# Kernel optimization log

Measured on AMD Instinct MI355X. Metric: run time of the kernel, lower is better.

## Reference

```python
import jax, jax.numpy as jnp
import numpy as np

N_NODES = 50000
N_EDGES = 800000
IN, HID, OUT = 256, 128, 64


def setup_inputs() -> dict:
    key = jax.random.key(0)
    ks = jax.random.split(key, 5)
    return {
        "x": jax.random.normal(ks[0], (N_NODES, IN), dtype=jnp.float32),
        "W1": jax.random.normal(ks[1], (IN, HID), dtype=jnp.float32) / np.sqrt(IN),
        "b1": jnp.zeros((HID,), dtype=jnp.float32),
        "W2": jax.random.normal(ks[2], (HID, OUT), dtype=jnp.float32) / np.sqrt(HID),
        "b2": jnp.zeros((OUT,), dtype=jnp.float32),
        "src": jax.random.randint(ks[3], (N_EDGES,), 0, N_NODES, dtype=jnp.int32),
        "dst": jax.random.randint(ks[4], (N_EDGES,), 0, N_NODES, dtype=jnp.int32),
    }


def _graph_conv(h, W, b, src, dst, norm_src, norm_dst, n_nodes):
    # DGL GraphConv, norm='both': y = D_dst^{-1/2} A D_src^{-1/2} h W + b
    # Project first (smaller feature dim for the SpMM), linearity makes it exact.
    h = h @ W                                     # [N, d_out]
    msg = (h * norm_src[:, None])[src]            # gather per-edge   [E, d_out]
    agg = jax.ops.segment_sum(msg, dst, num_segments=n_nodes)  # [N, d_out]
    return agg * norm_dst[:, None] + b


def reference(x, W1, b1, W2, b2, src, dst):
    n = x.shape[0]
    ones = jnp.ones(src.shape[0], dtype=jnp.float32)
    out_deg = jnp.zeros(n, jnp.float32).at[src].add(ones)
    in_deg = jnp.zeros(n, jnp.float32).at[dst].add(ones)
    norm_src = jax.lax.rsqrt(jnp.maximum(out_deg, 1.0))
    norm_dst = jax.lax.rsqrt(jnp.maximum(in_deg, 1.0))

    h = _graph_conv(x, W1, b1, src, dst, norm_src, norm_dst, n)
    h = jax.nn.relu(h)
    return _graph_conv(h, W2, b2, src, dst, norm_src, norm_dst, n)
```

## Files before the change

### kernel.cpp

```cpp
#include <hip/hip_runtime.h>

#define NN 50000
#define NE 800000
#define NPAD 50176
#define NSLICE 32
#define ESL 25000
#define HPN 25088
#define HPW 12544
#define FPN 12544
#define GB 782

typedef __attribute__((ext_vector_type(8))) short bf16x8;
typedef __attribute__((ext_vector_type(4))) float f32x4;

__device__ __forceinline__ float u2f(unsigned u) { return __uint_as_float(u); }
__device__ __forceinline__ unsigned f2u(float f) { return __float_as_uint(f); }
__device__ __forceinline__ unsigned short f2bf(float f) {
    unsigned u = f2u(f);
    return (unsigned short)((u + (((u >> 16) & 1u) + 0x7fffu)) >> 16);
}

__global__ __launch_bounds__(256) void wtrans_kernel(
    const float* __restrict__ W1, const float* __restrict__ W2,
    unsigned short* __restrict__ Wh1, unsigned short* __restrict__ Wl1,
    unsigned short* __restrict__ Wh2, unsigned short* __restrict__ Wl2) {
    int b = blockIdx.x;
    float w;
    unsigned short *ph, *pl;
    int f;
    if (b < 128) {
        int i = b * 256 + threadIdx.x;
        int k = i >> 7, n = i & 127;
        f = (((n >> 4) * 32 + (k >> 3)) * 16 + (n & 15)) * 8 + (k & 7);
        w = W1[i]; ph = Wh1; pl = Wl1;
    } else {
        int i = (b - 128) * 256 + threadIdx.x;
        int k = i >> 6, n = i & 63;
        f = (((n >> 4) * 16 + (k >> 3)) * 16 + (n & 15)) * 8 + (k & 7);
        w = W2[i]; ph = Wh2; pl = Wl2;
    }
    unsigned u = f2u(w);
    float lo = w - u2f(u & 0xffff0000u);
    ph[f] = (unsigned short)(u >> 16);
    pl[f] = (unsigned short)(f2u(lo) >> 16);
}

__global__ __launch_bounds__(1024) void hist_kernel(
    const int* __restrict__ src, const int* __restrict__ dst,
    unsigned* __restrict__ cnt_sl) {
    __shared__ unsigned lcnt[HPW];
    const int b = blockIdx.x;
    const int side = b & 1;
    const int slice = (b >> 1) & (NSLICE - 1);
    const int part = b >> 6;
    const int* __restrict__ arr = side ? dst : src;
    const int base = part * HPN;
    for (int j = threadIdx.x; j < HPW; j += 1024) lcnt[j] = 0;
    __syncthreads();
    const int e0 = slice * ESL;
    for (int i = e0 + threadIdx.x; i < e0 + ESL; i += 1024) {
        int v = arr[i] - base;
        if ((unsigned)v < (unsigned)HPN)
            atomicAdd(&lcnt[v >> 1], 1u << ((v & 1) * 16));
    }
    __syncthreads();
    unsigned* o = cnt_sl + (size_t)b * HPW;
    for (int j = threadIdx.x; j < HPW; j += 1024) o[j] = lcnt[j];
}

__global__ __launch_bounds__(256) void norm_scanA_kernel(
    const unsigned* __restrict__ cnt_sl, float* __restrict__ ns,
    float* __restrict__ nd, int* __restrict__ presum,
    int* __restrict__ pref, int* __restrict__ blk_sum, int n) {
    __shared__ int lds[256];
    int i = blockIdx.x * 256 + threadIdx.x;
    int d_total = 0;
    if (i < n) {
        int part = (i >= HPN) ? 1 : 0;
        int w = (i - part * HPN) >> 1;
        int sh = (i & 1) * 16;
        int s_total = 0;
#pragma unroll
        for (int sl = 0; sl < NSLICE; sl++) {
            int bb = part * 64 + sl * 2;
            s_total += (cnt_sl[(size_t)bb * HPW + w] >> sh) & 0xffff;
            int c = (cnt_sl[(size_t)(bb + 1) * HPW + w] >> sh) & 0xffff;
            presum[sl * NPAD + i] = d_total;
            d_total += c;
        }
        ns[i] = rsqrtf(fmaxf((float)s_total, 1.0f));
        nd[i] = rsqrtf(fmaxf((float)d_total, 1.0f));
    }
    lds[threadIdx.x] = d_total;
    __syncthreads();
    for (int ofs = 1; ofs < 256; ofs <<= 1) {
        int t = (threadIdx.x >= ofs) ? lds[threadIdx.x - ofs] : 0;
        __syncthreads();
        lds[threadIdx.x] += t;
        __syncthreads();
    }
    if (i < n) pref[i] = lds[threadIdx.x] - d_total;
    if (threadIdx.x == 255) blk_sum[blockIdx.x] = lds[255];
}

__global__ __launch_bounds__(256) void scanB_kernel(const int* __restrict__ blk_sum,
                                                    int* __restrict__ blk_ofs, int nb) {
    __shared__ int lds[256];
    int v = (threadIdx.x < nb) ? blk_sum[threadIdx.x] : 0;
    lds[threadIdx.x] = v;
    __syncthreads();
    for (int ofs = 1; ofs < 256; ofs <<= 1) {
        int t = (threadIdx.x >= ofs) ? lds[threadIdx.x - ofs] : 0;
        __syncthreads();
        lds[threadIdx.x] += t;
        __syncthreads();
    }
    if (threadIdx.x < nb) blk_ofs[threadIdx.x] = lds[threadIdx.x] - v;
}

__global__ __launch_bounds__(256) void scanC_kernel(int* __restrict__ row_ofs,
                                                    const int* __restrict__ blk_ofs, int n) {
    int i = blockIdx.x * 256 + threadIdx.x;
    if (i < n) row_ofs[i] += blk_ofs[blockIdx.x];
    if (i == 0) row_ofs[n] = NE;
}

__global__ __launch_bounds__(1024) void fill_kernel(
    const int* __restrict__ src, const int* __restrict__ dst,
    const int* __restrict__ row_ofs, const int* __restrict__ presum,
    int* __restrict__ eidx) {
    __shared__ int cur[FPN];
    const int slice = blockIdx.x >> 2;
    const int part = blockIdx.x & 3;
    const int base = part * FPN;
    for (int j = threadIdx.x; j < FPN; j += 1024) {
        int gi = base + j;
        cur[j] = (gi < NN) ? row_ofs[gi] + presum[slice * NPAD + gi] : 0;
    }
    __syncthreads();
    const int e0 = slice * ESL;
    for (int i = e0 + threadIdx.x; i < e0 + ESL; i += 1024) {
        int v = dst[i] - base;
        if ((unsigned)v < (unsigned)FPN) {
            int pos = atomicAdd(&cur[v], 1);
            eidx[pos] = src[i];
        }
    }
}

__global__ __launch_bounds__(256) void gemm1_kernel(
    const float* __restrict__ A, const unsigned short* __restrict__ Wh,
    const unsigned short* __restrict__ Wl, unsigned short* __restrict__ out, int M) {
    constexpr int N = 128, K = 256;
    constexpr int NT = N / 16, KC = K / 32;
    const int wave = threadIdx.x >> 6;
    const int lane = threadIdx.x & 63;
    const int ln = lane & 15;
    const int qk = lane >> 4;
    const int m0 = blockIdx.x * 64 + wave * 16;
    const int mA = m0 + ln;
    const bool a_ok = mA < M;
    const float* Arow = A + (size_t)(a_ok ? mA : (M - 1)) * K + qk * 8;
    const bf16x8* BH = (const bf16x8*)Wh;
    const bf16x8* BL = (const bf16x8*)Wl;

    f32x4 acc[NT];
#pragma unroll
    for (int t = 0; t < NT; t++) acc[t] = (f32x4){0.f, 0.f, 0.f, 0.f};

#pragma unroll 2
    for (int c = 0; c < KC; ++c) {
        float4 a0 = *(const float4*)(Arow + c * 32);
        float4 a1 = *(const float4*)(Arow + c * 32 + 4);
        float av[8] = {a0.x, a0.y, a0.z, a0.w, a1.x, a1.y, a1.z, a1.w};
        bf16x8 ah, al;
#pragma unroll
        for (int j = 0; j < 8; ++j) {
            unsigned u = f2u(av[j]);
            float lo = av[j] - u2f(u & 0xffff0000u);
            ah[j] = (short)(u >> 16);
            al[j] = (short)(f2u(lo) >> 16);
        }
        const int fb = c * 4 + qk;
#pragma unroll
        for (int t = 0; t < NT; ++t) {
            bf16x8 bh = BH[(t * (K / 8) + fb) * 16 + ln];
            bf16x8 bl = BL[(t * (K / 8) + fb) * 16 + ln];
            acc[t] = __builtin_amdgcn_mfma_f32_16x16x32_bf16(ah, bh, acc[t], 0, 0, 0);
            acc[t] = __builtin_amdgcn_mfma_f32_16x16x32_bf16(ah, bl, acc[t], 0, 0, 0);
            acc[t] = __builtin_amdgcn_mfma_f32_16x16x32_bf16(al, bh, acc[t], 0, 0, 0);
        }
    }
#pragma unroll
    for (int t = 0; t < NT; ++t)
#pragma unroll
        for (int r = 0; r < 4; ++r) {
            int row = m0 + qk * 4 + r;
            if (row < M) out[(size_t)row * N + t * 16 + ln] = f2bf(acc[t][r]);
        }
}

__global__ __launch_bounds__(256) void gemm2_kernel(
    const unsigned short* __restrict__ A, const unsigned short* __restrict__ Wh,
    const unsigned short* __restrict__ Wl, unsigned short* __restrict__ out, int M) {
    constexpr int N = 64, K = 128;
    constexpr int NT = N / 16, KC = K / 32;
    const int wave = threadIdx.x >> 6;
    const int lane = threadIdx.x & 63;
    const int ln = lane & 15;
    const int qk = lane >> 4;
    const int m0 = blockIdx.x * 64 + wave * 16;
    const int mA = m0 + ln;
    const unsigned short* Arow = A + (size_t)(mA < M ? mA : (M - 1)) * K + qk * 8;
    const bf16x8* BH = (const bf16x8*)Wh;
    const bf16x8* BL = (const bf16x8*)Wl;

    f32x4 acc[NT];
#pragma unroll
    for (int t = 0; t < NT; t++) acc[t] = (f32x4){0.f, 0.f, 0.f, 0.f};

#pragma unroll
    for (int c = 0; c < KC; ++c) {
        bf16x8 ah = *(const bf16x8*)(Arow + c * 32);
        const int fb = c * 4 + qk;
#pragma unroll
        for (int t = 0; t < NT; ++t) {
            bf16x8 bh = BH[(t * (K / 8) + fb) * 16 + ln];
            bf16x8 bl = BL[(t * (K / 8) + fb) * 16 + ln];
            acc[t] = __builtin_amdgcn_mfma_f32_16x16x32_bf16(ah, bh, acc[t], 0, 0, 0);
            acc[t] = __builtin_amdgcn_mfma_f32_16x16x32_bf16(ah, bl, acc[t], 0, 0, 0);
        }
    }
#pragma unroll
    for (int t = 0; t < NT; ++t)
#pragma unroll
        for (int r = 0; r < 4; ++r) {
            int row = m0 + qk * 4 + r;
            if (row < M) out[(size_t)row * N + t * 16 + ln] = f2bf(acc[t][r]);
        }
}

__global__ __launch_bounds__(256) void gather128_kernel(
    const unsigned* __restrict__ hs, const int* __restrict__ eidx,
    const int* __restrict__ row_ofs, const float* __restrict__ norm_src,
    const float* __restrict__ norm_dst, const float* __restrict__ bias,
    unsigned* __restrict__ out, int n) {
    int wave = (blockIdx.x * blockDim.x + threadIdx.x) >> 6;
    int lane = threadIdx.x & 63;
    if (wave >= n) return;
    int beg = row_ofs[wave], end = row_ofs[wave + 1];
    float sc = norm_dst[wave];
    float ax = 0.f, ay = 0.f;
    int e = beg;
    for (; e + 3 < end; e += 4) {
        int s0 = eidx[e], s1 = eidx[e + 1], s2 = eidx[e + 2], s3 = eidx[e + 3];
        float n0 = norm_src[s0], n1 = norm_src[s1];
        float n2 = norm_src[s2], n3 = norm_src[s3];
        unsigned u0 = hs[(size_t)s0 * 64 + lane];
        unsigned u1 = hs[(size_t)s1 * 64 + lane];
        unsigned u2 = hs[(size_t)s2 * 64 + lane];
        unsigned u3 = hs[(size_t)s3 * 64 + lane];
        ax += n0 * u2f(u0 << 16) + n1 * u2f(u1 << 16) +
              n2 * u2f(u2 << 16) + n3 * u2f(u3 << 16);
        ay += n0 * u2f(u0 & 0xffff0000u) + n1 * u2f(u1 & 0xffff0000u) +
              n2 * u2f(u2 & 0xffff0000u) + n3 * u2f(u3 & 0xffff0000u);
    }
    for (; e < end; ++e) {
        int s0 = eidx[e];
        float n0 = norm_src[s0];
        unsigned u0 = hs[(size_t)s0 * 64 + lane];
        ax += n0 * u2f(u0 << 16);
        ay += n0 * u2f(u0 & 0xffff0000u);
    }
    float2 b = ((const float2*)bias)[lane];
    float rx = fmaxf(ax * sc + b.x, 0.f);
    float ry = fmaxf(ay * sc + b.y, 0.f);
    out[(size_t)wave * 64 + lane] = (unsigned)f2bf(rx) | ((unsigned)f2bf(ry) << 16);
}

__global__ __launch_bounds__(256) void gather64_kernel(
    const unsigned* __restrict__ hs, const int* __restrict__ eidx,
    const int* __restrict__ row_ofs, const float* __restrict__ norm_src,
    const float* __restrict__ norm_dst, const float* __restrict__ bias,
    float* __restrict__ out, int n) {
    int wave = (blockIdx.x * blockDim.x + threadIdx.x) >> 6;
    int lane = threadIdx.x & 63;
    if (wave >= n) return;
    int beg = row_ofs[wave], end = row_ofs[wave + 1];
    int half = lane >> 5;
    int dim = lane & 31;
    float ax = 0.f, ay = 0.f;
    int e = beg + half;
    for (; e + 2 < end; e += 4) {
        int s0 = eidx[e], s1 = eidx[e + 2];
        float n0 = norm_src[s0], n1 = norm_src[s1];
        unsigned u0 = hs[(size_t)s0 * 32 + dim];
        unsigned u1 = hs[(size_t)s1 * 32 + dim];
        ax += n0 * u2f(u0 << 16) + n1 * u2f(u1 << 16);
        ay += n0 * u2f(u0 & 0xffff0000u) + n1 * u2f(u1 & 0xffff0000u);
    }
    if (e < end) {
        int s0 = eidx[e];
        float n0 = norm_src[s0];
        unsigned u0 = hs[(size_t)s0 * 32 + dim];
        ax += n0 * u2f(u0 << 16);
        ay += n0 * u2f(u0 & 0xffff0000u);
    }
    ax += __shfl_xor(ax, 32);
    ay += __shfl_xor(ay, 32);
    if (half == 0) {
        float sc = norm_dst[wave];
        float2 b = ((const float2*)bias)[dim];
        ((float2*)out)[(size_t)wave * 32 + dim] =
            make_float2(ax * sc + b.x, ay * sc + b.y);
    }
}

extern "C" void kernel_launch(void* const* d_in, const int* in_sizes, int n_in,
                              void* d_out, int out_size, void* d_ws, size_t ws_size,
                              hipStream_t stream) {
    const float* x  = (const float*)d_in[0];
    const float* W1 = (const float*)d_in[1];
    const float* b1 = (const float*)d_in[2];
    const float* W2 = (const float*)d_in[3];
    const float* b2 = (const float*)d_in[4];
    const int* src  = (const int*)d_in[5];
    const int* dst  = (const int*)d_in[6];
    float* out = (float*)d_out;
    char* ws = (char*)d_ws;

    const int NB = (NN + 255) / 256;

    float* norm_src = (float*)(ws);
    float* norm_dst = (float*)(ws + 4 * 50176);
    int*   row_ofs  = (int*)(ws + 4 * 100352);
    int*   blk_sum  = (int*)(ws + 4 * 150784);
    int*   blk_ofs  = (int*)(ws + 4 * 151040);
    int*   eidx     = (int*)(ws + 4 * 151296);
    unsigned short* Wh1 = (unsigned short*)(ws + 4 * 951296);
    unsigned short* Wl1 = (unsigned short*)(ws + 4 * 967680);
    unsigned short* Wh2 = (unsigned short*)(ws + 4 * 984064);
    unsigned short* Wl2 = (unsigned short*)(ws + 4 * 988160);
    unsigned short* hs1 = (unsigned short*)(ws + 4 * 992256);
    unsigned short* hs2 = (unsigned short*)(ws + 4 * 4192256);
    unsigned* cnt_sl    = (unsigned*)(ws + 4 * 5792256);
    int* presum         = (int*)(ws + 4 * 7397888);
    unsigned short* h1  = (unsigned short*)(ws + 4 * 5792256);

    wtrans_kernel<<<160, 256, 0, stream>>>(W1, W2, Wh1, Wl1, Wh2, Wl2);

    hist_kernel<<<128, 1024, 0, stream>>>(src, dst, cnt_sl);
    gemm1_kernel<<<GB, 256, 0, stream>>>(x, Wh1, Wl1, hs1, NN);

    norm_scanA_kernel<<<NB, 256, 0, stream>>>(cnt_sl, norm_src, norm_dst,
                                              presum, row_ofs, blk_sum, NN);
    scanB_kernel<<<1, 256, 0, stream>>>(blk_sum, blk_ofs, NB);
    scanC_kernel<<<NB, 256, 0, stream>>>(row_ofs, blk_ofs, NN);
    fill_kernel<<<128, 1024, 0, stream>>>(src, dst, row_ofs, presum, eidx);

    gather128_kernel<<<(NN + 3) / 4, 256, 0, stream>>>(
        (const unsigned*)hs1, eidx, row_ofs, norm_src, norm_dst, b1,
        (unsigned*)h1, NN);

    gemm2_kernel<<<GB, 256, 0, stream>>>(h1, Wh2, Wl2, hs2, NN);

    gather64_kernel<<<(NN + 3) / 4, 256, 0, stream>>>(
        (const unsigned*)hs2, eidx, row_ofs, norm_src, norm_dst, b2, out, NN);
}
```

Measured before the change: 240.2 us.

## Fuse layer-1 aggregation with layer-2 GEMM and merge scan kernels

Merges the three-stage row-offset scan into one kernel that uses a last-block-done atomic counter, and drops the separate offset-fixup pass. Readers now compute each row offset on the fly as pref plus blk_ofs. The layer-1 gather, ReLU and bf16 pack are fused with the layer-2 MFMA projection through shared memory, so the h1 intermediate no longer round-trips through global memory. This removes several launches and about 12.8 MB of traffic, at the cost of one wave per four nodes in the fused gather and an extra lookup per row boundary.

```diff
diff --git a/kernel.cpp b/kernel.cpp
--- a/kernel.cpp
+++ b/kernel.cpp
@@ -9,6 +9,7 @@
 #define HPW 12544
 #define FPN 12544
 #define GB 782
+#define NB 196
 
 typedef __attribute__((ext_vector_type(8))) short bf16x8;
 typedef __attribute__((ext_vector_type(4))) float f32x4;
@@ -23,7 +24,9 @@
 __global__ __launch_bounds__(256) void wtrans_kernel(
     const float* __restrict__ W1, const float* __restrict__ W2,
     unsigned short* __restrict__ Wh1, unsigned short* __restrict__ Wl1,
-    unsigned short* __restrict__ Wh2, unsigned short* __restrict__ Wl2) {
+    unsigned short* __restrict__ Wh2, unsigned short* __restrict__ Wl2,
+    int* __restrict__ done_cnt) {
+    if (blockIdx.x == 0 && threadIdx.x == 0) *done_cnt = 0;
     int b = blockIdx.x;
     float w;
     unsigned short *ph, *pl;
@@ -68,11 +71,13 @@
     for (int j = threadIdx.x; j < HPW; j += 1024) o[j] = lcnt[j];
 }
 
-__global__ __launch_bounds__(256) void norm_scanA_kernel(
+__global__ __launch_bounds__(256) void norm_scanAB_kernel(
     const unsigned* __restrict__ cnt_sl, float* __restrict__ ns,
     float* __restrict__ nd, int* __restrict__ presum,
-    int* __restrict__ pref, int* __restrict__ blk_sum, int n) {
+    int* __restrict__ pref, int* __restrict__ blk_sum,
+    int* __restrict__ blk_ofs, int* __restrict__ done_cnt, int n) {
     __shared__ int lds[256];
+    __shared__ int is_last;
     int i = blockIdx.x * 256 + threadIdx.x;
     int d_total = 0;
     if (i < n) {
@@ -101,12 +106,16 @@
     }
     if (i < n) pref[i] = lds[threadIdx.x] - d_total;
     if (threadIdx.x == 255) blk_sum[blockIdx.x] = lds[255];
-}
-
-__global__ __launch_bounds__(256) void scanB_kernel(const int* __restrict__ blk_sum,
-                                                    int* __restrict__ blk_ofs, int nb) {
-    __shared__ int lds[256];
-    int v = (threadIdx.x < nb) ? blk_sum[threadIdx.x] : 0;
+    __threadfence();
+    if (threadIdx.x == 0) {
+        int c = atomicAdd(done_cnt, 1);
+        is_last = (c == gridDim.x - 1);
+    }
+    __syncthreads();
+    if (!is_last) return;
+    __threadfence();
+    int v = (threadIdx.x < gridDim.x) ? blk_sum[threadIdx.x] : 0;
+    __syncthreads();
     lds[threadIdx.x] = v;
     __syncthreads();
     for (int ofs = 1; ofs < 256; ofs <<= 1) {
@@ -115,27 +124,20 @@
         lds[threadIdx.x] += t;
         __syncthreads();
     }
-    if (threadIdx.x < nb) blk_ofs[threadIdx.x] = lds[threadIdx.x] - v;
-}
-
-__global__ __launch_bounds__(256) void scanC_kernel(int* __restrict__ row_ofs,
-                                                    const int* __restrict__ blk_ofs, int n) {
-    int i = blockIdx.x * 256 + threadIdx.x;
-    if (i < n) row_ofs[i] += blk_ofs[blockIdx.x];
-    if (i == 0) row_ofs[n] = NE;
+    if (threadIdx.x < gridDim.x) blk_ofs[threadIdx.x] = lds[threadIdx.x] - v;
 }
 
 __global__ __launch_bounds__(1024) void fill_kernel(
     const int* __restrict__ src, const int* __restrict__ dst,
-    const int* __restrict__ row_ofs, const int* __restrict__ presum,
-    int* __restrict__ eidx) {
+    const int* __restrict__ pref, const int* __restrict__ blk_ofs,
+    const int* __restrict__ presum, int* __restrict__ eidx) {
     __shared__ int cur[FPN];
     const int slice = blockIdx.x >> 2;
     const int part = blockIdx.x & 3;
     const int base = part * FPN;
     for (int j = threadIdx.x; j < FPN; j += 1024) {
         int gi = base + j;
-        cur[j] = (gi < NN) ? row_ofs[gi] + presum[slice * NPAD + gi] : 0;
+        cur[j] = (gi < NN) ? pref[gi] + blk_ofs[gi >> 8] + presum[slice * NPAD + gi] : 0;
     }
     __syncthreads();
     const int e0 = slice * ESL;
@@ -159,8 +161,7 @@
     const int qk = lane >> 4;
     const int m0 = blockIdx.x * 64 + wave * 16;
     const int mA = m0 + ln;
-    const bool a_ok = mA < M;
-    const float* Arow = A + (size_t)(a_ok ? mA : (M - 1)) * K + qk * 8;
+    const float* Arow = A + (size_t)(mA < M ? mA : (M - 1)) * K + qk * 8;
     const bf16x8* BH = (const bf16x8*)Wh;
     const bf16x8* BL = (const bf16x8*)Wl;
 
@@ -200,93 +201,86 @@
         }
 }
 
-__global__ __launch_bounds__(256) void gemm2_kernel(
-    const unsigned short* __restrict__ A, const unsigned short* __restrict__ Wh,
-    const unsigned short* __restrict__ Wl, unsigned short* __restrict__ out, int M) {
-    constexpr int N = 64, K = 128;
-    constexpr int NT = N / 16, KC = K / 32;
+__global__ __launch_bounds__(256) void layer2_kernel(
+    const unsigned* __restrict__ hs1, const int* __restrict__ eidx,
+    const int* __restrict__ pref, const int* __restrict__ blk_ofs,
+    const float* __restrict__ norm_src, const float* __restrict__ norm_dst,
+    const float* __restrict__ bias, const unsigned short* __restrict__ Wh,
+    const unsigned short* __restrict__ Wl, unsigned short* __restrict__ hs2, int n) {
+    __shared__ unsigned lh1[16 * 68];
     const int wave = threadIdx.x >> 6;
     const int lane = threadIdx.x & 63;
+    const int nb = blockIdx.x * 16;
+
+    for (int j = 0; j < 4; ++j) {
+        const int node = nb + wave * 4 + j;
+        float rx = 0.f, ry = 0.f;
+        if (node < n) {
+            int beg = pref[node] + blk_ofs[node >> 8];
+            int end = (node + 1 < n) ? pref[node + 1] + blk_ofs[(node + 1) >> 8] : NE;
+            float ax = 0.f, ay = 0.f;
+            int e = beg;
+            for (; e + 3 < end; e += 4) {
+                int s0 = eidx[e], s1 = eidx[e + 1], s2 = eidx[e + 2], s3 = eidx[e + 3];
+                float n0 = norm_src[s0], n1 = norm_src[s1];
+                float n2 = norm_src[s2], n3 = norm_src[s3];
+                unsigned u0 = hs1[(size_t)s0 * 64 + lane];
+                unsigned u1 = hs1[(size_t)s1 * 64 + lane];
+                unsigned u2 = hs1[(size_t)s2 * 64 + lane];
+                unsigned u3 = hs1[(size_t)s3 * 64 + lane];
+                ax += n0 * u2f(u0 << 16) + n1 * u2f(u1 << 16) +
+                      n2 * u2f(u2 << 16) + n3 * u2f(u3 << 16);
+                ay += n0 * u2f(u0 & 0xffff0000u) + n1 * u2f(u1 & 0xffff0000u) +
+                      n2 * u2f(u2 & 0xffff0000u) + n3 * u2f(u3 & 0xffff0000u);
+            }
+            for (; e < end; ++e) {
+                int s0 = eidx[e];
+                float n0 = norm_src[s0];
+                unsigned u0 = hs1[(size_t)s0 * 64 + lane];
+                ax += n0 * u2f(u0 << 16);
+                ay += n0 * u2f(u0 & 0xffff0000u);
+            }
+            float sc = norm_dst[node];
+            float2 b = ((const float2*)bias)[lane];
+            rx = fmaxf(ax * sc + b.x, 0.f);
+            ry = fmaxf(ay * sc + b.y, 0.f);
+        }
+        lh1[(wave * 4 + j) * 68 + lane] = (unsigned)f2bf(rx) | ((unsigned)f2bf(ry) << 16);
+    }
+    __syncthreads();
+
     const int ln = lane & 15;
     const int qk = lane >> 4;
-    const int m0 = blockIdx.x * 64 + wave * 16;
-    const int mA = m0 + ln;
-    const unsigned short* Arow = A + (size_t)(mA < M ? mA : (M - 1)) * K + qk * 8;
+    const int t = wave;
     const bf16x8* BH = (const bf16x8*)Wh;
     const bf16x8* BL = (const bf16x8*)Wl;
-
-    f32x4 acc[NT];
-#pragma unroll
-    for (int t = 0; t < NT; t++) acc[t] = (f32x4){0.f, 0.f, 0.f, 0.f};
-
-#pragma unroll
-    for (int c = 0; c < KC; ++c) {
-        bf16x8 ah = *(const bf16x8*)(Arow + c * 32);
+    f32x4 acc = (f32x4){0.f, 0.f, 0.f, 0.f};
+#pragma unroll
+    for (int c = 0; c < 4; ++c) {
+        bf16x8 ah = *(const bf16x8*)&lh1[ln * 68 + c * 16 + qk * 4];
         const int fb = c * 4 + qk;
-#pragma unroll
-        for (int t = 0; t < NT; ++t) {
-            bf16x8 bh = BH[(t * (K / 8) + fb) * 16 + ln];
-            bf16x8 bl = BL[(t * (K / 8) + fb) * 16 + ln];
-            acc[t] = __builtin_amdgcn_mfma_f32_16x16x32_bf16(ah, bh, acc[t], 0, 0, 0);
-            acc[t] = __builtin_amdgcn_mfma_f32_16x16x32_bf16(ah, bl, acc[t], 0, 0, 0);
-        }
-    }
-#pragma unroll
-    for (int t = 0; t < NT; ++t)
-#pragma unroll
-        for (int r = 0; r < 4; ++r) {
-            int row = m0 + qk * 4 + r;
-            if (row < M) out[(size_t)row * N + t * 16 + ln] = f2bf(acc[t][r]);
-        }
-}
-
-__global__ __launch_bounds__(256) void gather128_kernel(
+        bf16x8 bh = BH[(t * 16 + fb) * 16 + ln];
+        bf16x8 bl = BL[(t * 16 + fb) * 16 + ln];
+        acc = __builtin_amdgcn_mfma_f32_16x16x32_bf16(ah, bh, acc, 0, 0, 0);
+        acc = __builtin_amdgcn_mfma_f32_16x16x32_bf16(ah, bl, acc, 0, 0, 0);
+    }
+#pragma unroll
+    for (int r = 0; r < 4; ++r) {
+        int node = nb + qk * 4 + r;
+        if (node < n) hs2[(size_t)node * 64 + t * 16 + ln] = f2bf(acc[r]);
+    }
+}
+
+__global__ __launch_bounds__(256) void gather64_kernel(
     const unsigned* __restrict__ hs, const int* __restrict__ eidx,
-    const int* __restrict__ row_ofs, const float* __restrict__ norm_src,
-    const float* __restrict__ norm_dst, const float* __restrict__ bias,
-    unsigned* __restrict__ out, int n) {
+    const int* __restrict__ pref, const int* __restrict__ blk_ofs,
+    const float* __restrict__ norm_src, const float* __restrict__ norm_dst,
+    const float* __restrict__ bias, float* __restrict__ out, int n) {
     int wave = (blockIdx.x * blockDim.x + threadIdx.x) >> 6;
     int lane = threadIdx.x & 63;
     if (wave >= n) return;
-    int beg = row_ofs[wave], end = row_ofs[wave + 1];
-    float sc = norm_dst[wave];
-    float ax = 0.f, ay = 0.f;
-    int e = beg;
-    for (; e + 3 < end; e += 4) {
-        int s0 = eidx[e], s1 = eidx[e + 1], s2 = eidx[e + 2], s3 = eidx[e + 3];
-        float n0 = norm_src[s0], n1 = norm_src[s1];
-        float n2 = norm_src[s2], n3 = norm_src[s3];
-        unsigned u0 = hs[(size_t)s0 * 64 + lane];
-        unsigned u1 = hs[(size_t)s1 * 64 + lane];
-        unsigned u2 = hs[(size_t)s2 * 64 + lane];
-        unsigned u3 = hs[(size_t)s3 * 64 + lane];
-        ax += n0 * u2f(u0 << 16) + n1 * u2f(u1 << 16) +
-              n2 * u2f(u2 << 16) + n3 * u2f(u3 << 16);
-        ay += n0 * u2f(u0 & 0xffff0000u) + n1 * u2f(u1 & 0xffff0000u) +
-              n2 * u2f(u2 & 0xffff0000u) + n3 * u2f(u3 & 0xffff0000u);
-    }
-    for (; e < end; ++e) {
-        int s0 = eidx[e];
-        float n0 = norm_src[s0];
-        unsigned u0 = hs[(size_t)s0 * 64 + lane];
-        ax += n0 * u2f(u0 << 16);
-        ay += n0 * u2f(u0 & 0xffff0000u);
-    }
-    float2 b = ((const float2*)bias)[lane];
-    float rx = fmaxf(ax * sc + b.x, 0.f);
-    float ry = fmaxf(ay * sc + b.y, 0.f);
-    out[(size_t)wave * 64 + lane] = (unsigned)f2bf(rx) | ((unsigned)f2bf(ry) << 16);
-}
-
-__global__ __launch_bounds__(256) void gather64_kernel(
-    const unsigned* __restrict__ hs, const int* __restrict__ eidx,
-    const int* __restrict__ row_ofs, const float* __restrict__ norm_src,
-    const float* __restrict__ norm_dst, const float* __restrict__ bias,
-    float* __restrict__ out, int n) {
-    int wave = (blockIdx.x * blockDim.x + threadIdx.x) >> 6;
-    int lane = threadIdx.x & 63;
-    if (wave >= n) return;
-    int beg = row_ofs[wave], end = row_ofs[wave + 1];
+    int beg = pref[wave] + blk_ofs[wave >> 8];
+    int end = (wave + 1 < n) ? pref[wave + 1] + blk_ofs[(wave + 1) >> 8] : NE;
     int half = lane >> 5;
     int dim = lane & 31;
     float ax = 0.f, ay = 0.f;
@@ -329,13 +323,12 @@
     float* out = (float*)d_out;
     char* ws = (char*)d_ws;
 
-    const int NB = (NN + 255) / 256;
-
     float* norm_src = (float*)(ws);
     float* norm_dst = (float*)(ws + 4 * 50176);
-    int*   row_ofs  = (int*)(ws + 4 * 100352);
-    int*   blk_sum  = (int*)(ws + 4 * 150784);
-    int*   blk_ofs  = (int*)(ws + 4 * 151040);
+    int*   pref     = (int*)(ws + 4 * 100352);
+    int*   blk_sum  = (int*)(ws + 4 * 150528);
+    int*   blk_ofs  = (int*)(ws + 4 * 150784);
+    int*   done_cnt = (int*)(ws + 4 * 151040);
     int*   eidx     = (int*)(ws + 4 * 151296);
     unsigned short* Wh1 = (unsigned short*)(ws + 4 * 951296);
     unsigned short* Wl1 = (unsigned short*)(ws + 4 * 967680);
@@ -345,25 +338,21 @@
     unsigned short* hs2 = (unsigned short*)(ws + 4 * 4192256);
     unsigned* cnt_sl    = (unsigned*)(ws + 4 * 5792256);
     int* presum         = (int*)(ws + 4 * 7397888);
-    unsigned short* h1  = (unsigned short*)(ws + 4 * 5792256);
-
-    wtrans_kernel<<<160, 256, 0, stream>>>(W1, W2, Wh1, Wl1, Wh2, Wl2);
+
+    wtrans_kernel<<<160, 256, 0, stream>>>(W1, W2, Wh1, Wl1, Wh2, Wl2, done_cnt);
 
     hist_kernel<<<128, 1024, 0, stream>>>(src, dst, cnt_sl);
     gemm1_kernel<<<GB, 256, 0, stream>>>(x, Wh1, Wl1, hs1, NN);
 
-    norm_scanA_kernel<<<NB, 256, 0, stream>>>(cnt_sl, norm_src, norm_dst,
-                                              presum, row_ofs, blk_sum, NN);
-    scanB_kernel<<<1, 256, 0, stream>>>(blk_sum, blk_ofs, NB);
-    scanC_kernel<<<NB, 256, 0, stream>>>(row_ofs, blk_ofs, NN);
-    fill_kernel<<<128, 1024, 0, stream>>>(src, dst, row_ofs, presum, eidx);
-
-    gather128_kernel<<<(NN + 3) / 4, 256, 0, stream>>>(
-        (const unsigned*)hs1, eidx, row_ofs, norm_src, norm_dst, b1,
-        (unsigned*)h1, NN);
-
-    gemm2_kernel<<<GB, 256, 0, stream>>>(h1, Wh2, Wl2, hs2, NN);
-
-    gather64_kernel<<<(NN + 3) / 4, 256, 0, stream>>>(
-        (const unsigned*)hs2, eidx, row_ofs, norm_src, norm_dst, b2, out, NN);
-}
+    norm_scanAB_kernel<<<NB, 256, 0, stream>>>(cnt_sl, norm_src, norm_dst,
+                                               presum, pref, blk_sum, blk_ofs,
+                                               done_cnt, NN);
+    fill_kernel<<<128, 1024, 0, stream>>>(src, dst, pref, blk_ofs, presum, eidx);
+
+    layer2_kernel<<<3125, 256, 0, stream>>>(
+        (const unsigned*)hs1, eidx, pref, blk_ofs, norm_src, norm_dst, b1,
+        Wh2, Wl2, hs2, NN);
+
+    gather64_kernel<<<12500, 256, 0, stream>>>(
+        (const unsigned*)hs2, eidx, pref, blk_ofs, norm_src, norm_dst, b2, out, NN);
+}
```

Result: slower. 250.9 us (+4.5%).
